# Optimization experiments

Measured on AMD Instinct MI355X. Metric: run time of the kernel, lower is better.

The kernel has to match this reference:

```python
import jax, jax.numpy as jnp
import numpy as np

B, S, C, T = 256, 128, 64, 60
ENC, COL, RNN, ATT, ACT, TYP = 512, 512, 512, 512, 128, 64
NPROD, NTYPE = 97, 32
LS, PTEMP, CTEMP = 0.2, 1.0, 1.0
NEG = -1e9


def setup_inputs() -> dict:
    key = jax.random.key(0)
    ks = jax.random.split(key, 24)
    enc = jax.random.normal(ks[0], (B, S, ENC), jnp.float32)
    col_enc = jax.random.normal(ks[1], (B, C, COL), jnp.float32)
    enc_lens = jax.random.randint(ks[2], (B,), 1, S + 1)
    col_lens = jax.random.randint(ks[3], (B,), 1, C + 1)
    action_kind = jax.random.randint(ks[4], (B, T), 0, 3)  # 0=ApplyRule,1=Reduce,2=SelectColumn
    tgt_lens = jax.random.randint(ks[5], (B,), 1, T + 1)
    prod_ids = jax.random.randint(ks[6], (B, T), 0, NPROD)
    col_ids = jax.random.randint(ks[7], (B, T), 0, C) % col_lens[:, None]
    parent_prod = jax.random.randint(ks[8], (B, T), 0, NPROD)
    parent_type = jax.random.randint(ks[9], (B, T), 0, NTYPE)
    parent_time = jax.random.randint(ks[10], (B, T), 0, T) % jnp.maximum(jnp.arange(T), 1)[None, :]
    g = lambda k, shp: jax.random.normal(k, shp, jnp.float32) * 0.02
    IN = ACT + ATT + ACT + TYP + RNN  # a_tm1 | att_tm1 | parent_prod | parent_type | parent_h
    return dict(
        enc=enc, col_enc=col_enc, enc_lens=enc_lens, col_lens=col_lens,
        action_kind=action_kind, tgt_lens=tgt_lens, prod_ids=prod_ids,
        col_ids=col_ids, parent_prod=parent_prod, parent_type=parent_type,
        parent_time=parent_time,
        prod_embed=g(ks[11], (NPROD + 1, ACT)),
        type_embed=g(ks[12], (NTYPE, TYP)),
        b_lin=jnp.zeros((NPROD + 1,), jnp.float32),
        W_ih=g(ks[13], (IN, 4 * RNN)), W_hh=g(ks[14], (RNN, 4 * RNN)),
        b_lstm=jnp.zeros((4 * RNN,), jnp.float32),
        W_att_q=g(ks[15], (RNN, ENC)),
        W_att_vec=g(ks[16], (ENC + RNN, ATT)),
        W_r1=g(ks[17], (ATT, 4 * ATT)), b_r1=jnp.zeros((4 * ATT,), jnp.float32),
        W_r2=g(ks[18], (4 * ATT, ACT)), b_r2=jnp.zeros((ACT,), jnp.float32),
        W_col_in=g(ks[19], (COL, ACT)),
        W_ptr=g(ks[20], (ATT, COL)),
        w_mem=g(ks[21], (ATT, 1)),
    )


def reference(enc, col_enc, enc_lens, col_lens, action_kind, tgt_lens, prod_ids,
              col_ids, parent_prod, parent_type, parent_time,
              prod_embed, type_embed, b_lin, W_ih, W_hh, b_lstm,
              W_att_q, W_att_vec, W_r1, b_r1, W_r2, b_r2,
              W_col_in, W_ptr, w_mem):
    enc_mask = jnp.arange(S)[None, :] < enc_lens[:, None]   # [B,S]
    col_valid = jnp.arange(C)[None, :] < col_lens[:, None]  # [B,C]
    col_in_embed = jnp.einsum('bcd,da->bca', col_enc, W_col_in)  # column_rnn_input, [B,C,ACT]

    # previous-step actions (a_{t-1}); dummy zeros at t=0 (x is zeroed there anyway)
    shift = lambda a: jnp.concatenate([jnp.zeros_like(a[:, :1]), a[:, :-1]], axis=1)
    kind_p, pid_p, cid_p = shift(action_kind), shift(prod_ids), shift(col_ids)

    def scan_step(carry, xs):
        h, c, att, hist, appear, acc = carry
        t, kp, pp, cp, kind, pid, cid, fprod, ftype, ptime = xs
        # --- prep step input ---
        prev_valid = (t - 1) < tgt_lens
        e_rule = prod_embed[jnp.where(kp == 1, NPROD, pp)]                      # [B,ACT]
        e_col = jnp.take_along_axis(col_in_embed, cp[:, None, None], axis=1)[:, 0]
        a_embed = jnp.where((kp == 2)[:, None], e_col, e_rule)
        a_embed = jnp.where(prev_valid[:, None], a_embed, 0.0)
        parent_h = hist[ptime, jnp.arange(B)]                                   # [B,RNN]
        x = jnp.concatenate([a_embed, att, prod_embed[fprod], type_embed[ftype], parent_h], axis=-1)
        x = jnp.where(t == 0, 0.0, x)
        # --- LSTMCell (torch gate order i,f,g,o) ---
        gates = x @ W_ih + h @ W_hh + b_lstm
        i, f, g_, o = jnp.split(gates, 4, axis=-1)
        c_new = jax.nn.sigmoid(f) * c + jax.nn.sigmoid(i) * jnp.tanh(g_)
        h_new = jax.nn.sigmoid(o) * jnp.tanh(c_new)
        # --- attention over encoder ---
        scores = jnp.einsum('bd,bsd->bs', h_new @ W_att_q, enc)
        scores = jnp.where(enc_mask, scores, NEG)
        ctx = jnp.einsum('bs,bsd->bd', jax.nn.softmax(scores, axis=-1), enc)
        att_new = jnp.tanh(jnp.concatenate([ctx, h_new], axis=-1) @ W_att_vec)
        # --- production readout (tied output embedding) ---
        emb_q = jnp.tanh(att_new @ W_r1 + b_r1) @ W_r2 + b_r2
        rule_lp = jax.nn.log_softmax((emb_q @ prod_embed.T + b_lin) / PTEMP, axis=-1)
        # --- pointer net over columns with memory gate ---
        gate = jax.nn.sigmoid(att_new @ w_mem)                                  # [B,1]
        w_c = jnp.einsum('bd,bcd->bc', att_new @ W_ptr, col_enc)
        weights = w_c * appear * gate + w_c * (1.0 - appear) * (1.0 - gate)
        weights = jnp.where(col_valid, weights, NEG) / CTEMP
        col_lp = jax.nn.log_softmax(weights, axis=-1)
        # --- per-example log prob of gold action ---
        valid = t < tgt_lens
        lp_rule = jnp.take_along_axis(rule_lp, jnp.where(kind == 1, NPROD, pid)[:, None], axis=1)[:, 0]
        lp_col_raw = jnp.take_along_axis(col_lp, cid[:, None], axis=1)[:, 0]
        col_sum = jnp.sum(jnp.where(col_valid, col_lp, 0.0), axis=-1)
        lp_col = (1.0 - LS) * lp_col_raw + LS * col_sum / col_lens
        lp = jnp.where(kind == 2, lp_col, lp_rule)
        acc = acc + jnp.where(valid, lp, 0.0)
        # --- state updates (appear mask updated after use, matching torch) ---
        appear = jnp.maximum(appear, ((kind == 2) & valid)[:, None] * jax.nn.one_hot(cid, C, dtype=appear.dtype))
        hist = hist.at[t].set(h_new)
        return (h_new, c_new, att_new, hist, appear, acc), None

    carry0 = (
        jnp.zeros((B, RNN), jnp.float32), jnp.zeros((B, RNN), jnp.float32),
        jnp.zeros((B, ATT), jnp.float32), jnp.zeros((T, B, RNN), jnp.float32),
        jnp.zeros((B, C), jnp.float32), jnp.zeros((B,), jnp.float32),
    )
    xs = (jnp.arange(T), kind_p.T, pid_p.T, cid_p.T, action_kind.T, prod_ids.T,
          col_ids.T, parent_prod.T, parent_type.T, parent_time.T)
    (_, _, _, _, _, acc), _ = jax.lax.scan(scan_step, carry0, xs)
    return -jnp.mean(acc)
```

## Files before the change

### kernel.cpp

```cpp
#include <hip/hip_runtime.h>
#include <math.h>

#define NB 256
#define NS 128
#define NCOL 64
#define NT 60
#define DENC 512
#define DRNN 512
#define DATT 512
#define DACT 128
#define DTYP 64
#define DG 2048
#define NEGV (-1e9f)
#define NBH 131072
#define NROW 15360
#define RPW 576
#define NRP 2624

typedef unsigned short ushort_t;
typedef __attribute__((ext_vector_type(8))) short short8;
typedef __attribute__((ext_vector_type(4))) float f32x4;

__device__ __forceinline__ float sigf(float x) { return 1.0f / (1.0f + __expf(-x)); }
__device__ __forceinline__ float tanhfast(float x) {
  x = fminf(fmaxf(x, -15.0f), 15.0f);
  float e = __expf(-2.0f * x);
  return (1.0f - e) / (1.0f + e);
}
__device__ __forceinline__ ushort_t f2bf(float f) {
  union { float f; unsigned u; } v; v.f = f;
  unsigned r = v.u + 0x7fffu + ((v.u >> 16) & 1u);
  return (ushort_t)(r >> 16);
}
__device__ __forceinline__ float bf2f(ushort_t b) {
  union { unsigned u; float f; } v; v.u = ((unsigned)b) << 16; return v.f;
}
__device__ __forceinline__ void ld8(const float* p, float* d) {
  f32x4 x = *(const f32x4*)p, y = *(const f32x4*)(p + 4);
  d[0]=x[0]; d[1]=x[1]; d[2]=x[2]; d[3]=x[3];
  d[4]=y[0]; d[5]=y[1]; d[6]=y[2]; d[7]=y[3];
}
__device__ __forceinline__ short8 cvt8(const float* p) {
  f32x4 x = *(const f32x4*)p, y = *(const f32x4*)(p + 4);
  short8 r;
  r[0]=(short)f2bf(x[0]); r[1]=(short)f2bf(x[1]); r[2]=(short)f2bf(x[2]); r[3]=(short)f2bf(x[3]);
  r[4]=(short)f2bf(y[0]); r[5]=(short)f2bf(y[1]); r[6]=(short)f2bf(y[2]); r[7]=(short)f2bf(y[3]);
  return r;
}

__global__ __launch_bounds__(256) void zero_kernel(float* __restrict__ p, int n) {
  int i = blockIdx.x * 256 + threadIdx.x;
  if (i < n) p[i] = 0.0f;
}

__global__ __launch_bounds__(256) void cvt_bf16_kernel(const float* __restrict__ src,
    ushort_t* __restrict__ dst, int n8)
{
  int i = blockIdx.x * 256 + threadIdx.x;
  if (i < n8) *(short8*)&dst[(size_t)i * 8] = cvt8(src + (size_t)i * 8);
}

__global__ __launch_bounds__(256) void pack_w(const float* __restrict__ src,
    ushort_t* __restrict__ dst, int Ksub, int Nsub, int Ntot, int K0, int N0, int ldsrc)
{
  int idx = blockIdx.x * 256 + threadIdx.x;
  if (idx >= Ksub * Nsub) return;
  int k = idx / Nsub, n = idx - k * Nsub;
  int gk = K0 + k;
  dst[((size_t)(gk >> 3) * Ntot + (N0 + n)) * 8 + (gk & 7)] =
      f2bf(src[(size_t)k * ldsrc + n]);
}

__global__ __launch_bounds__(256) void pack_wT(const float* __restrict__ W,
    ushort_t* __restrict__ dst)
{
  int idx = blockIdx.x * 256 + threadIdx.x;
  if (idx >= 512 * 512) return;
  int r = idx >> 9, d = idx & 511;
  dst[((size_t)(d >> 3) * 512 + r) * 8 + (d & 7)] = f2bf(W[(size_t)r * 512 + d]);
}

__global__ __launch_bounds__(256) void r2p_kernel(const float* __restrict__ W_r2,
    const float* __restrict__ prod_embed, const float* __restrict__ b_r2,
    const float* __restrict__ b_lin, ushort_t* __restrict__ Wr2p,
    float* __restrict__ bias2)
{
  int idx = blockIdx.x * 256 + threadIdx.x;
  if (idx >= 2049 * 98) return;
  int k = idx / 98, j = idx - k * 98;
  const float* pe = prod_embed + (size_t)j * DACT;
  if (k < 2048) {
    const float* wr = W_r2 + (size_t)k * DACT;
    float a = 0.f;
    #pragma unroll 8
    for (int d = 0; d < DACT; ++d) a = fmaf(wr[d], pe[d], a);
    Wr2p[((size_t)(k >> 3) * 128 + j) * 8 + (k & 7)] = f2bf(a);
  } else {
    float a = b_lin[j];
    #pragma unroll 8
    for (int d = 0; d < DACT; ++d) a = fmaf(b_r2[d], pe[d], a);
    bias2[j] = a;
  }
}

__global__ __launch_bounds__(64) void appear_kernel(const int* __restrict__ action_kind,
    const int* __restrict__ tgt_lens, const int* __restrict__ col_ids,
    float* __restrict__ appear_all)
{
  int b = blockIdx.x, c = threadIdx.x;
  float ap = 0.f;
  int tl = tgt_lens[b];
  for (int t = 0; t < NT; ++t) {
    appear_all[((size_t)t * NB + b) * 64 + c] = ap;
    if (t < tl && action_kind[b * NT + t] == 2 && col_ids[b * NT + t] == c) ap = 1.f;
  }
}

__global__ __launch_bounds__(256) void gemm_bf16(
    const float* __restrict__ A1, int lda1,
    const ushort_t* __restrict__ Bp, ushort_t* __restrict__ Cb, int ldc,
    int N, int K)
{
  __shared__ short As[2][4096];
  __shared__ short Bs[2][4096];
  const int tid = threadIdx.x;
  const int lane = tid & 63, w = tid >> 6;
  const int wr = w >> 1, wc = w & 1;
  const int mBase = blockIdx.y * 64, nBase = blockIdx.x * 64;
  const int nt = K >> 6;
  f32x4 ra0[2], ra1[2];
  short8 rb[2];
  auto issue = [&](int kt) {
    #pragma unroll
    for (int s = 0; s < 2; ++s) {
      int slot = tid + s * 256;
      int kc = slot >> 6, m = slot & 63;
      int k0 = (kt << 6) + kc * 8;
      const float* p = A1 + (size_t)(mBase + m) * lda1 + k0;
      ra0[s] = *(const f32x4*)p;
      ra1[s] = *(const f32x4*)(p + 4);
      rb[s] = *(const short8*)(Bp + ((size_t)(k0 >> 3) * N + nBase + m) * 8);
    }
  };
  auto store = [&](int buf) {
    #pragma unroll
    for (int s = 0; s < 2; ++s) {
      int slot = tid + s * 256;
      short8 av;
      av[0]=(short)f2bf(ra0[s][0]); av[1]=(short)f2bf(ra0[s][1]);
      av[2]=(short)f2bf(ra0[s][2]); av[3]=(short)f2bf(ra0[s][3]);
      av[4]=(short)f2bf(ra1[s][0]); av[5]=(short)f2bf(ra1[s][1]);
      av[6]=(short)f2bf(ra1[s][2]); av[7]=(short)f2bf(ra1[s][3]);
      *(short8*)&As[buf][slot * 8] = av;
      *(short8*)&Bs[buf][slot * 8] = rb[s];
    }
  };
  f32x4 z4 = {0.f,0.f,0.f,0.f};
  f32x4 acc[2][2] = {{z4,z4},{z4,z4}};
  issue(0); store(0);
  __syncthreads();
  int cur = 0;
  for (int kt = 0; kt < nt; ++kt) {
    bool more = (kt + 1 < nt);
    if (more) issue(kt + 1);
    #pragma unroll
    for (int kk = 0; kk < 2; ++kk) {
      int ko = kk * 4 + (lane >> 4);
      short8 af[2], bfr[2];
      #pragma unroll
      for (int f = 0; f < 2; ++f) {
        int row = wr * 32 + f * 16 + (lane & 15);
        af[f] = *(const short8*)&As[cur][(ko * 64 + row) * 8];
        int col = wc * 32 + f * 16 + (lane & 15);
        bfr[f] = *(const short8*)&Bs[cur][(ko * 64 + col) * 8];
      }
      #pragma unroll
      for (int i = 0; i < 2; ++i)
        #pragma unroll
        for (int j = 0; j < 2; ++j)
          acc[i][j] = __builtin_amdgcn_mfma_f32_16x16x32_bf16(af[i], bfr[j], acc[i][j], 0, 0, 0);
    }
    if (more) store(cur ^ 1);
    __syncthreads();
    cur ^= 1;
  }
  #pragma unroll
  for (int i = 0; i < 2; ++i)
    #pragma unroll
    for (int j = 0; j < 2; ++j)
      #pragma unroll
      for (int r = 0; r < 4; ++r) {
        int row = mBase + wr * 32 + i * 16 + (lane >> 4) * 4 + r;
        int col = nBase + wc * 32 + j * 16 + (lane & 15);
        Cb[(size_t)row * ldc + col] = f2bf(acc[i][j][r]);
      }
}

template <class FA, class FB, class FE>
__device__ __forceinline__ void gemm_core(char* smem, FA loadA, FB loadB,
    int ktBeg, int ktEnd, FE epi)
{
  short* As = (short*)smem;
  short* Bs = (short*)smem + 8192;
  const int tid = threadIdx.x;
  const int lane = tid & 63, w = tid >> 6;
  const int wr = w >> 1, wc = w & 1;
  f32x4 z4 = {0.f,0.f,0.f,0.f};
  f32x4 acc[2][2] = {{z4,z4},{z4,z4}};
  short8 pa[2], pb[2];
  auto issue = [&](int kt) {
    #pragma unroll
    for (int s = 0; s < 2; ++s) {
      int slot = tid + s * 256;
      int kc = slot >> 6;
      int k = (kt << 6) + (kc << 3);
      pa[s] = loadA(k);
      pb[s] = loadB(slot & 63, k);
    }
  };
  auto store = [&](int buf) {
    #pragma unroll
    for (int s = 0; s < 2; ++s) {
      int slot = tid + s * 256;
      *(short8*)&As[buf * 4096 + slot * 8] = pa[s];
      *(short8*)&Bs[buf * 4096 + slot * 8] = pb[s];
    }
  };
  issue(ktBeg); store(0);
  __syncthreads();
  int cur = 0;
  for (int kt = ktBeg; kt < ktEnd; ++kt) {
    bool more = (kt + 1 < ktEnd);
    if (more) issue(kt + 1);
    #pragma unroll
    for (int kk = 0; kk < 2; ++kk) {
      int ko = kk * 4 + (lane >> 4);
      short8 af[2], bfr[2];
      #pragma unroll
      for (int f = 0; f < 2; ++f) {
        int row = wr * 32 + f * 16 + (lane & 15);
        af[f] = *(const short8*)&As[cur * 4096 + (ko * 64 + row) * 8];
        int col = wc * 32 + f * 16 + (lane & 15);
        bfr[f] = *(const short8*)&Bs[cur * 4096 + (ko * 64 + col) * 8];
      }
      #pragma unroll
      for (int i = 0; i < 2; ++i)
        #pragma unroll
        for (int j = 0; j < 2; ++j)
          acc[i][j] = __builtin_amdgcn_mfma_f32_16x16x32_bf16(af[i], bfr[j], acc[i][j], 0, 0, 0);
    }
    if (more) store(cur ^ 1);
    __syncthreads();
    cur ^= 1;
  }
  #pragma unroll
  for (int i = 0; i < 2; ++i)
    #pragma unroll
    for (int j = 0; j < 2; ++j)
      #pragma unroll
      for (int r = 0; r < 4; ++r) {
        int rl = wr * 32 + i * 16 + (lane >> 4) * 4 + r;
        int cl = wc * 32 + j * 16 + (lane & 15);
        epi(rl, cl, acc[i][j][r]);
      }
}

__global__ __launch_bounds__(256) void k1_gates(
    const int* __restrict__ action_kind, const int* __restrict__ tgt_lens,
    const int* __restrict__ prod_ids, const int* __restrict__ col_ids,
    const int* __restrict__ parent_prod, const int* __restrict__ parent_type,
    const int* __restrict__ parent_time,
    const float* __restrict__ prod_embed, const float* __restrict__ type_embed,
    const ushort_t* __restrict__ WpG, const ushort_t* __restrict__ colin_b,
    const ushort_t* __restrict__ att_all, const ushort_t* __restrict__ hist_u,
    float* __restrict__ gates0, float* __restrict__ gates1, int t)
{
  __shared__ __align__(16) char smem[32768];
  const int tid = threadIdx.x;
  const int nb = blockIdx.x, mb = blockIdx.y, ks = blockIdx.z;
  const int mBase = mb * 64, nBase = nb * 64;
  const int b = mBase + (tid & 63);
  int kp = action_kind[b * NT + t - 1];
  int pp = prod_ids[b * NT + t - 1];
  int cp = col_ids[b * NT + t - 1];
  bool pv = (t - 1) < tgt_lens[b];
  int fp = parent_prod[b * NT + t];
  int ft = parent_type[b * NT + t];
  int ptm = parent_time[b * NT + t];
  const ushort_t* hist_prev = hist_u + (size_t)(t - 1) * NBH;
  const ushort_t* att_prev = att_all + (size_t)(t - 1) * NB * DATT;
  auto loadA = [&](int k) -> short8 {
    short8 z = {0,0,0,0,0,0,0,0};
    if (k < 128) {
      if (!pv) return z;
      if (kp == 2) return *(const short8*)(colin_b + ((size_t)(b * NCOL + cp) * DACT + k));
      int row = (kp == 1) ? 97 : pp;
      return cvt8(prod_embed + (size_t)row * DACT + k);
    } else if (k < 640) {
      return *(const short8*)(att_prev + (size_t)b * DATT + (k - 128));
    } else if (k < 768) {
      return cvt8(prod_embed + (size_t)fp * DACT + (k - 640));
    } else if (k < 832) {
      return cvt8(type_embed + (size_t)ft * DTYP + (k - 768));
    } else if (k < 1344) {
      return *(const short8*)(hist_u + (size_t)ptm * NBH + (size_t)b * DRNN + (k - 832));
    } else {
      return *(const short8*)(hist_prev + (size_t)b * DRNN + (k - 1344));
    }
  };
  auto loadB = [&](int n, int k) -> short8 {
    return *(const short8*)(WpG + ((size_t)(k >> 3) * DG + nBase + n) * 8);
  };
  float* gp = ks ? gates1 : gates0;
  auto epi = [&](int rl, int cl, float v) {
    gp[(size_t)(mBase + rl) * DG + nBase + cl] = v;
  };
  gemm_core(smem, loadA, loadB, ks ? 15 : 0, ks ? 29 : 15, epi);
}

struct SmemK23 { float hq[DRNN]; float ml[4][2]; float cs[4][DENC]; };
__global__ __launch_bounds__(256) void k23_lstm_attn(
    const float* __restrict__ g0, const float* __restrict__ g1,
    const float* __restrict__ b_lstm, float* __restrict__ cst,
    ushort_t* __restrict__ hist_t,
    const ushort_t* __restrict__ encWq, const float* __restrict__ enc,
    const int* __restrict__ enc_lens, ushort_t* __restrict__ ctxb)
{
  __shared__ __align__(16) SmemK23 s;
  int b = blockIdx.x, tid = threadIdx.x;
  #pragma unroll
  for (int r = 0; r < 2; ++r) {
    int j = tid + r * 256;
    const float* p0 = g0 + (size_t)b * DG;
    const float* p1 = g1 + (size_t)b * DG;
    float gi = p0[j]        + p1[j]        + b_lstm[j];
    float gf = p0[512 + j]  + p1[512 + j]  + b_lstm[512 + j];
    float gg = p0[1024 + j] + p1[1024 + j] + b_lstm[1024 + j];
    float go = p0[1536 + j] + p1[1536 + j] + b_lstm[1536 + j];
    size_t ix = (size_t)b * DRNN + j;
    float cn = sigf(gf) * cst[ix] + sigf(gi) * tanhfast(gg);
    float hn = sigf(go) * tanhfast(cn);
    cst[ix] = cn;
    hist_t[ix] = f2bf(hn);
    s.hq[j] = hn;
  }
  __syncthreads();
  int w = tid >> 6, lane = tid & 63;
  int el = enc_lens[b];
  float q[8];
  #pragma unroll
  for (int j = 0; j < 8; ++j) q[j] = s.hq[lane * 8 + j];
  float m = -1e30f, lr = 0.f;
  float cacc[8];
  #pragma unroll
  for (int j = 0; j < 8; ++j) cacc[j] = 0.f;
  const ushort_t* eWb = encWq + (size_t)b * NS * DENC + lane * 8;
  const float* eb = enc + (size_t)b * NS * DENC + lane * 8;
  for (int sI = w; sI < el; sI += 4) {
    short8 xr = *(const short8*)(eWb + (size_t)sI * DENC);
    float ev[8];
    ld8(eb + (size_t)sI * DENC, ev);
    float d = 0.f;
    #pragma unroll
    for (int j = 0; j < 8; ++j) d = fmaf(bf2f((ushort_t)xr[j]), q[j], d);
    #pragma unroll
    for (int off = 32; off > 0; off >>= 1) d += __shfl_xor(d, off);
    float mn = fmaxf(m, d);
    float rr = __expf(m - mn), p = __expf(d - mn);
    lr = lr * rr + p;
    #pragma unroll
    for (int j = 0; j < 8; ++j) cacc[j] = cacc[j] * rr + p * ev[j];
    m = mn;
  }
  if (lane == 0) { s.ml[w][0] = m; s.ml[w][1] = lr; }
  #pragma unroll
  for (int j = 0; j < 8; ++j) s.cs[w][lane * 8 + j] = cacc[j];
  __syncthreads();
  float M = fmaxf(fmaxf(s.ml[0][0], s.ml[1][0]), fmaxf(s.ml[2][0], s.ml[3][0]));
  float f0 = __expf(s.ml[0][0] - M), f1 = __expf(s.ml[1][0] - M);
  float f2 = __expf(s.ml[2][0] - M), f3 = __expf(s.ml[3][0] - M);
  float invL = 1.f / (f0 * s.ml[0][1] + f1 * s.ml[1][1] + f2 * s.ml[2][1] + f3 * s.ml[3][1]);
  #pragma unroll
  for (int rep = 0; rep < 2; ++rep) {
    int d = tid + rep * 256;
    ctxb[(size_t)b * DENC + d] =
        f2bf((f0 * s.cs[0][d] + f1 * s.cs[1][d] + f2 * s.cs[2][d] + f3 * s.cs[3][d]) * invL);
  }
}

__global__ __launch_bounds__(256) void k4_attvec(const ushort_t* __restrict__ ctxb,
    const ushort_t* __restrict__ hist_t, const ushort_t* __restrict__ WpV,
    ushort_t* __restrict__ att_all, int t)
{
  __shared__ __align__(16) char smem[32768];
  const int tid = threadIdx.x;
  const int mBase = blockIdx.y * 64, nBase = blockIdx.x * 64;
  const int b = mBase + (tid & 63);
  auto loadA = [&](int k) -> short8 {
    if (k < 512) return *(const short8*)(ctxb + (size_t)b * DENC + k);
    return *(const short8*)(hist_t + (size_t)b * DRNN + (k - 512));
  };
  auto loadB = [&](int n, int k) -> short8 {
    return *(const short8*)(WpV + ((size_t)(k >> 3) * 512 + nBase + n) * 8);
  };
  auto epi = [&](int rl, int cl, float v) {
    att_all[((size_t)t * NB + mBase + rl) * DATT + nBase + cl] = f2bf(tanhfast(v));
  };
  gemm_core(smem, loadA, loadB, 0, 16, epi);
}

__global__ __launch_bounds__(256) void kbig_r1ptr(const ushort_t* __restrict__ att_all,
    const ushort_t* __restrict__ WpRP, const float* __restrict__ b_r1,
    ushort_t* __restrict__ r1c, ushort_t* __restrict__ ptrq_all,
    float* __restrict__ gate_all, int rowBase)
{
  __shared__ __align__(16) char smem[32768];
  const int tid = threadIdx.x;
  const int mBase = blockIdx.y * 64, nBase = blockIdx.x * 64;
  const size_t grow = (size_t)rowBase + mBase + (tid & 63);
  auto loadA = [&](int k) -> short8 {
    return *(const short8*)(att_all + grow * DATT + k);
  };
  auto loadB = [&](int n, int k) -> short8 {
    return *(const short8*)(WpRP + ((size_t)(k >> 3) * NRP + nBase + n) * 8);
  };
  auto epi = [&](int rl, int cl, float v) {
    int col = nBase + cl;
    size_t gr = (size_t)rowBase + mBase + rl;
    if (col < 2048)      r1c[(size_t)(mBase + rl) * DG + col] = f2bf(tanhfast(v + b_r1[col]));
    else if (col < 2560) ptrq_all[gr * RPW + (col - 2048)] = f2bf(v);
    else if (col == 2560) gate_all[gr] = v;
  };
  gemm_core(smem, loadA, loadB, 0, 8, epi);
}

__global__ __launch_bounds__(256) void klogits(const ushort_t* __restrict__ r1c,
    const ushort_t* __restrict__ Wr2p, float* __restrict__ logits_all, int rowBase)
{
  __shared__ __align__(16) char smem[32768];
  const int tid = threadIdx.x;
  const int mBase = blockIdx.y * 64, nBase = blockIdx.x * 64;
  auto loadA = [&](int k) -> short8 {
    return *(const short8*)(r1c + (size_t)(mBase + (tid & 63)) * DG + k);
  };
  auto loadB = [&](int n, int k) -> short8 {
    return *(const short8*)(Wr2p + ((size_t)(k >> 3) * 128 + nBase + n) * 8);
  };
  auto epi = [&](int rl, int cl, float v) {
    logits_all[((size_t)rowBase + mBase + rl) * 128 + nBase + cl] = v;
  };
  gemm_core(smem, loadA, loadB, 0, 32, epi);
}

__global__ __launch_bounds__(256) void kwc(const ushort_t* __restrict__ ptrq_all,
    const ushort_t* __restrict__ colenc_b, float* __restrict__ w_c_all)
{
  __shared__ __align__(16) char smem[32768];
  const int tid = threadIdx.x;
  const int b = blockIdx.x;
  const int tt = tid & 63;
  auto loadA = [&](int k) -> short8 {
    short8 z = {0,0,0,0,0,0,0,0};
    if (tt >= NT) return z;
    return *(const short8*)(ptrq_all + ((size_t)tt * NB + b) * RPW + k);
  };
  auto loadB = [&](int n, int k) -> short8 {
    return *(const short8*)(colenc_b + ((size_t)b * NCOL + n) * 512 + k);
  };
  auto epi = [&](int rl, int cl, float v) {
    if (rl < NT) w_c_all[((size_t)rl * NB + b) * 64 + cl] = v;
  };
  gemm_core(smem, loadA, loadB, 0, 8, epi);
}

__global__ __launch_bounds__(64) void kfinal(
    const float* __restrict__ logits_all, const float* __restrict__ bias2,
    const float* __restrict__ w_c_all, const float* __restrict__ gate_all,
    const float* __restrict__ appear_all, const int* __restrict__ col_lens,
    const int* __restrict__ tgt_lens, const int* __restrict__ action_kind,
    const int* __restrict__ prod_ids, const int* __restrict__ col_ids,
    float* __restrict__ loss_tb)
{
  int row = blockIdx.x;
  int t = row >> 8, b = row & 255;
  int c = threadIdx.x;
  float l0 = logits_all[(size_t)row * 128 + c] + bias2[c];
  float l1 = (c + 64 < 98) ? logits_all[(size_t)row * 128 + 64 + c] + bias2[64 + c] : -1e30f;
  float m = fmaxf(l0, l1);
  #pragma unroll
  for (int off = 32; off > 0; off >>= 1) m = fmaxf(m, __shfl_down(m, off));
  m = __shfl(m, 0);
  float sv = __expf(l0 - m) + ((c + 64 < 98) ? __expf(l1 - m) : 0.f);
  #pragma unroll
  for (int off = 32; off > 0; off >>= 1) sv += __shfl_down(sv, off);
  sv = __shfl(sv, 0);
  float lseR = m + __logf(sv);
  int clen = col_lens[b];
  float gate = sigf(gate_all[row]);
  float ap = appear_all[(size_t)row * 64 + c];
  float wc = w_c_all[(size_t)row * 64 + c];
  float wv = wc * (ap * gate + (1.f - ap) * (1.f - gate));
  wv = (c < clen) ? wv : NEGV;
  float m2 = wv;
  #pragma unroll
  for (int off = 32; off > 0; off >>= 1) m2 = fmaxf(m2, __shfl_down(m2, off));
  m2 = __shfl(m2, 0);
  float s2 = __expf(wv - m2);
  #pragma unroll
  for (int off = 32; off > 0; off >>= 1) s2 += __shfl_down(s2, off);
  s2 = __shfl(s2, 0);
  float lse2 = m2 + __logf(s2);
  float csum = (c < clen) ? (wv - lse2) : 0.f;
  #pragma unroll
  for (int off = 32; off > 0; off >>= 1) csum += __shfl_down(csum, off);
  int kind = action_kind[b * NT + t];
  int cid = col_ids[b * NT + t];
  float wcid = __shfl(wv, cid);
  if (c == 0) {
    int pid = prod_ids[b * NT + t];
    bool valid = t < tgt_lens[b];
    int gj = (kind == 1) ? 97 : pid;
    float lgj = logits_all[(size_t)row * 128 + gj] + bias2[gj];
    float lp_rule = lgj - lseR;
    float lp_col = 0.8f * (wcid - lse2) + 0.2f * csum / (float)clen;
    float lp = (kind == 2) ? lp_col : lp_rule;
    loss_tb[row] = valid ? lp : 0.f;
  }
}

__global__ __launch_bounds__(256) void loss_reduce(const float* __restrict__ loss_tb,
                                                   float* __restrict__ out) {
  int tid = threadIdx.x;
  float v = 0.f;
  for (int k = 0; k < NT; ++k) v += loss_tb[(size_t)k * NB + tid];
  #pragma unroll
  for (int off = 32; off > 0; off >>= 1) v += __shfl_down(v, off);
  __shared__ float part[4];
  if ((tid & 63) == 0) part[tid >> 6] = v;
  __syncthreads();
  if (tid == 0) out[0] = -(part[0] + part[1] + part[2] + part[3]) * (1.0f / NB);
}

extern "C" void kernel_launch(void* const* d_in, const int* in_sizes, int n_in,
                              void* d_out, int out_size, void* d_ws, size_t ws_size,
                              hipStream_t stream) {
  const float* enc         = (const float*)d_in[0];
  const float* col_enc     = (const float*)d_in[1];
  const int*   enc_lens    = (const int*)d_in[2];
  const int*   col_lens    = (const int*)d_in[3];
  const int*   action_kind = (const int*)d_in[4];
  const int*   tgt_lens    = (const int*)d_in[5];
  const int*   prod_ids    = (const int*)d_in[6];
  const int*   col_ids     = (const int*)d_in[7];
  const int*   parent_prod = (const int*)d_in[8];
  const int*   parent_type = (const int*)d_in[9];
  const int*   parent_time = (const int*)d_in[10];
  const float* prod_embed  = (const float*)d_in[11];
  const float* type_embed  = (const float*)d_in[12];
  const float* b_lin       = (const float*)d_in[13];
  const float* W_ih        = (const float*)d_in[14];
  const float* W_hh        = (const float*)d_in[15];
  const float* b_lstm      = (const float*)d_in[16];
  const float* W_att_q     = (const float*)d_in[17];
  const float* W_att_vec   = (const float*)d_in[18];
  const float* W_r1        = (const float*)d_in[19];
  const float* b_r1        = (const float*)d_in[20];
  const float* W_r2        = (const float*)d_in[21];
  const float* b_r2        = (const float*)d_in[22];
  const float* W_col_in    = (const float*)d_in[23];
  const float* W_ptr       = (const float*)d_in[24];
  const float* w_mem       = (const float*)d_in[25];

  float* base = (float*)d_ws;
  size_t o = 0;
  float* cst    = base + o; o += 131072;
  float* gates0 = base + o; o += 524288;
  float* gates1 = base + o; o += 524288;
  int zeroN = (int)o;
  ushort_t* hist_u = (ushort_t*)(base + o); o += 3932160;
  float* logits_all = (float*)hist_u;
  ushort_t* colin_b = (ushort_t*)(base + o); o += 1048576;
  ushort_t* ctxb    = (ushort_t*)(base + o); o += 65536;
  float* encWq_f    = base + o; o += 8388608;
  ushort_t* encWq   = (ushort_t*)encWq_f;
  ushort_t* colenc_b = (ushort_t*)encWq_f;
  ushort_t* r1c      = (ushort_t*)(encWq_f + 4194304);
  ushort_t* att_all  = (ushort_t*)(base + o); o += 3932160;
  ushort_t* ptrq_all = (ushort_t*)(base + o); o += 4423680;
  float* gate_all    = base + o; o += 15360;
  float* w_c_all     = base + o; o += 983040;
  float* appear_all  = base + o; o += 983040;
  float* loss_tb     = base + o; o += 15360;
  ushort_t* WpG   = (ushort_t*)(base + o); o += 1900544;
  ushort_t* WqTp  = (ushort_t*)(base + o); o += 131072;
  ushort_t* WpV   = (ushort_t*)(base + o); o += 262144;
  ushort_t* WpRP  = (ushort_t*)(base + o); o += 671744;
  ushort_t* WpCI  = (ushort_t*)(base + o); o += 32768;
  ushort_t* Wr2p  = (ushort_t*)(base + o); o += 131072;
  float* bias2    = base + o; o += 128;
  (void)ws_size; (void)in_sizes; (void)n_in; (void)out_size;

  zero_kernel<<<(zeroN + 255) / 256, 256, 0, stream>>>(base, zeroN);
  zero_kernel<<<(671744 + 255) / 256, 256, 0, stream>>>((float*)WpRP, 671744);
  zero_kernel<<<(131072 + 255) / 256, 256, 0, stream>>>((float*)Wr2p, 131072);

  pack_w<<<(1344 * 2048 + 255) / 256, 256, 0, stream>>>(W_ih, WpG, 1344, 2048, 2048, 0, 0, 2048);
  pack_w<<<(512 * 2048 + 255) / 256, 256, 0, stream>>>(W_hh, WpG, 512, 2048, 2048, 1344, 0, 2048);
  pack_wT<<<(512 * 512 + 255) / 256, 256, 0, stream>>>(W_att_q, WqTp);
  pack_w<<<(1024 * 512 + 255) / 256, 256, 0, stream>>>(W_att_vec, WpV, 1024, 512, 512, 0, 0, 512);
  pack_w<<<(512 * 2048 + 255) / 256, 256, 0, stream>>>(W_r1, WpRP, 512, 2048, NRP, 0, 0, 2048);
  pack_w<<<(512 * 512 + 255) / 256, 256, 0, stream>>>(W_ptr, WpRP, 512, 512, NRP, 0, 2048, 512);
  pack_w<<<(512 + 255) / 256, 256, 0, stream>>>(w_mem, WpRP, 512, 1, NRP, 0, 2560, 1);
  pack_w<<<(512 * 128 + 255) / 256, 256, 0, stream>>>(W_col_in, WpCI, 512, 128, 128, 0, 0, 128);
  r2p_kernel<<<(2049 * 98 + 255) / 256, 256, 0, stream>>>(W_r2, prod_embed, b_r2, b_lin, Wr2p, bias2);
  appear_kernel<<<NB, 64, 0, stream>>>(action_kind, tgt_lens, col_ids, appear_all);

  gemm_bf16<<<dim3(2, 256), 256, 0, stream>>>(col_enc, 512, WpCI, colin_b, 128, 128, 512);
  gemm_bf16<<<dim3(8, 512), 256, 0, stream>>>(enc, 512, WqTp, encWq, 512, 512, 512);

  for (int t = 0; t < NT; ++t) {
    ushort_t* hist_t = hist_u + (size_t)t * NBH;
    if (t > 0)
      k1_gates<<<dim3(32, 4, 2), 256, 0, stream>>>(
          action_kind, tgt_lens, prod_ids, col_ids, parent_prod, parent_type,
          parent_time, prod_embed, type_embed, WpG, colin_b, att_all, hist_u,
          gates0, gates1, t);
    k23_lstm_attn<<<NB, 256, 0, stream>>>(gates0, gates1, b_lstm, cst, hist_t,
                                          encWq, enc, enc_lens, ctxb);
    k4_attvec<<<dim3(8, 4), 256, 0, stream>>>(ctxb, hist_t, WpV, att_all, t);
  }

  cvt_bf16_kernel<<<(1048576 + 255) / 256, 256, 0, stream>>>(col_enc, colenc_b, 1048576);
  for (int ch = 0; ch < 4; ++ch) {
    int rowBase = ch * 3840;
    kbig_r1ptr<<<dim3(41, 60), 256, 0, stream>>>(att_all, WpRP, b_r1, r1c,
                                                 ptrq_all, gate_all, rowBase);
    klogits<<<dim3(2, 60), 256, 0, stream>>>(r1c, Wr2p, logits_all, rowBase);
  }
  kwc<<<NB, 256, 0, stream>>>(ptrq_all, colenc_b, w_c_all);
  kfinal<<<NROW, 64, 0, stream>>>(logits_all, bias2, w_c_all, gate_all,
      appear_all, col_lens, tgt_lens, action_kind, prod_ids, col_ids, loss_tb);
  loss_reduce<<<1, 256, 0, stream>>>(loss_tb, (float*)d_out);
}
```

Baseline: 3.496 ms.

## Fuse attention-vector projection into LSTM/attention kernel and split gate GEMM four ways

```diff
diff --git a/kernel.cpp b/kernel.cpp
--- a/kernel.cpp
+++ b/kernel.cpp
@@ -80,6 +80,15 @@
   dst[((size_t)(d >> 3) * 512 + r) * 8 + (d & 7)] = f2bf(W[(size_t)r * 512 + d]);
 }
 
+__global__ __launch_bounds__(256) void pack_wvT(const float* __restrict__ W,
+    ushort_t* __restrict__ dst)
+{
+  int idx = blockIdx.x * 256 + threadIdx.x;
+  if (idx >= 1024 * 512) return;
+  int k = idx >> 9, j = idx & 511;
+  dst[(size_t)j * 1024 + k] = f2bf(W[(size_t)k * 512 + j]);
+}
+
 __global__ __launch_bounds__(256) void r2p_kernel(const float* __restrict__ W_r2,
     const float* __restrict__ prod_embed, const float* __restrict__ b_r2,
     const float* __restrict__ b_lin, ushort_t* __restrict__ Wr2p,
@@ -196,6 +205,59 @@
       }
 }
 
+__global__ __launch_bounds__(256) void gemm_encwq(
+    const float* __restrict__ enc, const ushort_t* __restrict__ WqTp,
+    ushort_t* __restrict__ encWq)
+{
+  __shared__ short Asm[32768];
+  const int tid = threadIdx.x;
+  const int lane = tid & 63, w = tid >> 6;
+  const int wr = w >> 1, wc = w & 1;
+  const int mBase = blockIdx.x * 64;
+  #pragma unroll
+  for (int it = 0; it < 16; ++it) {
+    int o = tid + it * 256;
+    int row = o >> 6, c = o & 63;
+    short8 v = cvt8(enc + (size_t)(mBase + row) * 512 + c * 8);
+    *(short8*)&Asm[row * 512 + ((c ^ (row & 7)) * 8)] = v;
+  }
+  __syncthreads();
+  for (int nt = 0; nt < 8; ++nt) {
+    f32x4 z4 = {0.f,0.f,0.f,0.f};
+    f32x4 acc[2][2] = {{z4,z4},{z4,z4}};
+    #pragma unroll 2
+    for (int kt = 0; kt < 8; ++kt) {
+      #pragma unroll
+      for (int kk = 0; kk < 2; ++kk) {
+        int ko = kt * 8 + kk * 4 + (lane >> 4);
+        short8 af[2], bfr[2];
+        #pragma unroll
+        for (int f = 0; f < 2; ++f) {
+          int row = wr * 32 + f * 16 + (lane & 15);
+          af[f] = *(const short8*)&Asm[row * 512 + ((ko ^ (row & 7)) * 8)];
+          int col = nt * 64 + wc * 32 + f * 16 + (lane & 15);
+          bfr[f] = *(const short8*)(WqTp + ((size_t)ko * 512 + col) * 8);
+        }
+        #pragma unroll
+        for (int i = 0; i < 2; ++i)
+          #pragma unroll
+          for (int j = 0; j < 2; ++j)
+            acc[i][j] = __builtin_amdgcn_mfma_f32_16x16x32_bf16(af[i], bfr[j], acc[i][j], 0, 0, 0);
+      }
+    }
+    #pragma unroll
+    for (int i = 0; i < 2; ++i)
+      #pragma unroll
+      for (int j = 0; j < 2; ++j)
+        #pragma unroll
+        for (int r = 0; r < 4; ++r) {
+          int row = mBase + wr * 32 + i * 16 + (lane >> 4) * 4 + r;
+          int col = nt * 64 + wc * 32 + j * 16 + (lane & 15);
+          encWq[(size_t)row * 512 + col] = f2bf(acc[i][j][r]);
+        }
+  }
+}
+
 template <class FA, class FB, class FE>
 __device__ __forceinline__ void gemm_core(char* smem, FA loadA, FB loadB,
     int ktBeg, int ktEnd, FE epi)
@@ -273,7 +335,8 @@
     const float* __restrict__ prod_embed, const float* __restrict__ type_embed,
     const ushort_t* __restrict__ WpG, const ushort_t* __restrict__ colin_b,
     const ushort_t* __restrict__ att_all, const ushort_t* __restrict__ hist_u,
-    float* __restrict__ gates0, float* __restrict__ gates1, int t)
+    float* __restrict__ gates0, float* __restrict__ gates1,
+    float* __restrict__ gates2, float* __restrict__ gates3, int t)
 {
   __shared__ __align__(16) char smem[32768];
   const int tid = threadIdx.x;
@@ -311,45 +374,51 @@
   auto loadB = [&](int n, int k) -> short8 {
     return *(const short8*)(WpG + ((size_t)(k >> 3) * DG + nBase + n) * 8);
   };
-  float* gp = ks ? gates1 : gates0;
+  float* gp = (ks == 0) ? gates0 : (ks == 1) ? gates1 : (ks == 2) ? gates2 : gates3;
   auto epi = [&](int rl, int cl, float v) {
     gp[(size_t)(mBase + rl) * DG + nBase + cl] = v;
   };
-  gemm_core(smem, loadA, loadB, ks ? 15 : 0, ks ? 29 : 15, epi);
-}
-
-struct SmemK23 { float hq[DRNN]; float ml[4][2]; float cs[4][DENC]; };
-__global__ __launch_bounds__(256) void k23_lstm_attn(
+  const int kb0 = (ks == 0) ? 0 : (ks == 1) ? 8 : (ks == 2) ? 15 : 22;
+  const int kb1 = (ks == 0) ? 8 : (ks == 1) ? 15 : (ks == 2) ? 22 : 29;
+  gemm_core(smem, loadA, loadB, kb0, kb1, epi);
+}
+
+struct SmemK23 { float ctxh[1024]; float ml[4][2]; float cs[4][DENC]; };
+__global__ __launch_bounds__(256) void k23_fused(
     const float* __restrict__ g0, const float* __restrict__ g1,
+    const float* __restrict__ g2, const float* __restrict__ g3,
     const float* __restrict__ b_lstm, float* __restrict__ cst,
     ushort_t* __restrict__ hist_t,
     const ushort_t* __restrict__ encWq, const float* __restrict__ enc,
-    const int* __restrict__ enc_lens, ushort_t* __restrict__ ctxb)
+    const int* __restrict__ enc_lens, const ushort_t* __restrict__ WvT,
+    ushort_t* __restrict__ att_t)
 {
   __shared__ __align__(16) SmemK23 s;
   int b = blockIdx.x, tid = threadIdx.x;
+  const float* p0 = g0 + (size_t)b * DG;
+  const float* p1 = g1 + (size_t)b * DG;
+  const float* p2 = g2 + (size_t)b * DG;
+  const float* p3 = g3 + (size_t)b * DG;
   #pragma unroll
   for (int r = 0; r < 2; ++r) {
     int j = tid + r * 256;
-    const float* p0 = g0 + (size_t)b * DG;
-    const float* p1 = g1 + (size_t)b * DG;
-    float gi = p0[j]        + p1[j]        + b_lstm[j];
-    float gf = p0[512 + j]  + p1[512 + j]  + b_lstm[512 + j];
-    float gg = p0[1024 + j] + p1[1024 + j] + b_lstm[1024 + j];
-    float go = p0[1536 + j] + p1[1536 + j] + b_lstm[1536 + j];
+    float gi = p0[j] + p1[j] + p2[j] + p3[j] + b_lstm[j];
+    float gf = p0[512+j] + p1[512+j] + p2[512+j] + p3[512+j] + b_lstm[512+j];
+    float gg = p0[1024+j] + p1[1024+j] + p2[1024+j] + p3[1024+j] + b_lstm[1024+j];
+    float go = p0[1536+j] + p1[1536+j] + p2[1536+j] + p3[1536+j] + b_lstm[1536+j];
     size_t ix = (size_t)b * DRNN + j;
     float cn = sigf(gf) * cst[ix] + sigf(gi) * tanhfast(gg);
     float hn = sigf(go) * tanhfast(cn);
     cst[ix] = cn;
     hist_t[ix] = f2bf(hn);
-    s.hq[j] = hn;
+    s.ctxh[512 + j] = hn;
   }
   __syncthreads();
   int w = tid >> 6, lane = tid & 63;
   int el = enc_lens[b];
   float q[8];
   #pragma unroll
-  for (int j = 0; j < 8; ++j) q[j] = s.hq[lane * 8 + j];
+  for (int j = 0; j < 8; ++j) q[j] = s.ctxh[512 + lane * 8 + j];
   float m = -1e30f, lr = 0.f;
   float cacc[8];
   #pragma unroll
@@ -383,30 +452,23 @@
   #pragma unroll
   for (int rep = 0; rep < 2; ++rep) {
     int d = tid + rep * 256;
-    ctxb[(size_t)b * DENC + d] =
-        f2bf((f0 * s.cs[0][d] + f1 * s.cs[1][d] + f2 * s.cs[2][d] + f3 * s.cs[3][d]) * invL);
-  }
-}
-
-__global__ __launch_bounds__(256) void k4_attvec(const ushort_t* __restrict__ ctxb,
-    const ushort_t* __restrict__ hist_t, const ushort_t* __restrict__ WpV,
-    ushort_t* __restrict__ att_all, int t)
-{
-  __shared__ __align__(16) char smem[32768];
-  const int tid = threadIdx.x;
-  const int mBase = blockIdx.y * 64, nBase = blockIdx.x * 64;
-  const int b = mBase + (tid & 63);
-  auto loadA = [&](int k) -> short8 {
-    if (k < 512) return *(const short8*)(ctxb + (size_t)b * DENC + k);
-    return *(const short8*)(hist_t + (size_t)b * DRNN + (k - 512));
-  };
-  auto loadB = [&](int n, int k) -> short8 {
-    return *(const short8*)(WpV + ((size_t)(k >> 3) * 512 + nBase + n) * 8);
-  };
-  auto epi = [&](int rl, int cl, float v) {
-    att_all[((size_t)t * NB + mBase + rl) * DATT + nBase + cl] = f2bf(tanhfast(v));
-  };
-  gemm_core(smem, loadA, loadB, 0, 16, epi);
+    s.ctxh[d] = (f0 * s.cs[0][d] + f1 * s.cs[1][d] + f2 * s.cs[2][d] + f3 * s.cs[3][d]) * invL;
+  }
+  __syncthreads();
+  #pragma unroll
+  for (int r = 0; r < 2; ++r) {
+    int j = tid + r * 256;
+    const short8* wp = (const short8*)(WvT + (size_t)j * 1024);
+    float a = 0.f;
+    #pragma unroll 4
+    for (int u = 0; u < 128; ++u) {
+      short8 wv = wp[u];
+      #pragma unroll
+      for (int e = 0; e < 8; ++e)
+        a = fmaf(bf2f((ushort_t)wv[e]), s.ctxh[u * 8 + e], a);
+    }
+    att_t[(size_t)b * DATT + j] = f2bf(tanhfast(a));
+  }
 }
 
 __global__ __launch_bounds__(256) void kbig_r1ptr(const ushort_t* __restrict__ att_all,
@@ -576,11 +638,12 @@
   float* cst    = base + o; o += 131072;
   float* gates0 = base + o; o += 524288;
   float* gates1 = base + o; o += 524288;
+  float* gates2 = base + o; o += 524288;
+  float* gates3 = base + o; o += 524288;
   int zeroN = (int)o;
   ushort_t* hist_u = (ushort_t*)(base + o); o += 3932160;
   float* logits_all = (float*)hist_u;
   ushort_t* colin_b = (ushort_t*)(base + o); o += 1048576;
-  ushort_t* ctxb    = (ushort_t*)(base + o); o += 65536;
   float* encWq_f    = base + o; o += 8388608;
   ushort_t* encWq   = (ushort_t*)encWq_f;
   ushort_t* colenc_b = (ushort_t*)encWq_f;
@@ -593,7 +656,7 @@
   float* loss_tb     = base + o; o += 15360;
   ushort_t* WpG   = (ushort_t*)(base + o); o += 1900544;
   ushort_t* WqTp  = (ushort_t*)(base + o); o += 131072;
-  ushort_t* WpV   = (ushort_t*)(base + o); o += 262144;
+  ushort_t* WvT   = (ushort_t*)(base + o); o += 262144;
   ushort_t* WpRP  = (ushort_t*)(base + o); o += 671744;
   ushort_t* WpCI  = (ushort_t*)(base + o); o += 32768;
   ushort_t* Wr2p  = (ushort_t*)(base + o); o += 131072;
@@ -607,7 +670,7 @@
   pack_w<<<(1344 * 2048 + 255) / 256, 256, 0, stream>>>(W_ih, WpG, 1344, 2048, 2048, 0, 0, 2048);
   pack_w<<<(512 * 2048 + 255) / 256, 256, 0, stream>>>(W_hh, WpG, 512, 2048, 2048, 1344, 0, 2048);
   pack_wT<<<(512 * 512 + 255) / 256, 256, 0, stream>>>(W_att_q, WqTp);
-  pack_w<<<(1024 * 512 + 255) / 256, 256, 0, stream>>>(W_att_vec, WpV, 1024, 512, 512, 0, 0, 512);
+  pack_wvT<<<(1024 * 512 + 255) / 256, 256, 0, stream>>>(W_att_vec, WvT);
   pack_w<<<(512 * 2048 + 255) / 256, 256, 0, stream>>>(W_r1, WpRP, 512, 2048, NRP, 0, 0, 2048);
   pack_w<<<(512 * 512 + 255) / 256, 256, 0, stream>>>(W_ptr, WpRP, 512, 512, NRP, 0, 2048, 512);
   pack_w<<<(512 + 255) / 256, 256, 0, stream>>>(w_mem, WpRP, 512, 1, NRP, 0, 2560, 1);
@@ -616,18 +679,18 @@
   appear_kernel<<<NB, 64, 0, stream>>>(action_kind, tgt_lens, col_ids, appear_all);
 
   gemm_bf16<<<dim3(2, 256), 256, 0, stream>>>(col_enc, 512, WpCI, colin_b, 128, 128, 512);
-  gemm_bf16<<<dim3(8, 512), 256, 0, stream>>>(enc, 512, WqTp, encWq, 512, 512, 512);
+  gemm_encwq<<<512, 256, 0, stream>>>(enc, WqTp, encWq);
 
   for (int t = 0; t < NT; ++t) {
     ushort_t* hist_t = hist_u + (size_t)t * NBH;
     if (t > 0)
-      k1_gates<<<dim3(32, 4, 2), 256, 0, stream>>>(
+      k1_gates<<<dim3(32, 4, 4), 256, 0, stream>>>(
           action_kind, tgt_lens, prod_ids, col_ids, parent_prod, parent_type,
           parent_time, prod_embed, type_embed, WpG, colin_b, att_all, hist_u,
-          gates0, gates1, t);
-    k23_lstm_attn<<<NB, 256, 0, stream>>>(gates0, gates1, b_lstm, cst, hist_t,
-                                          encWq, enc, enc_lens, ctxb);
-    k4_attvec<<<dim3(8, 4), 256, 0, stream>>>(ctxb, hist_t, WpV, att_all, t);
+          gates0, gates1, gates2, gates3, t);
+    k23_fused<<<NB, 256, 0, stream>>>(gates0, gates1, gates2, gates3, b_lstm,
+        cst, hist_t, encWq, enc, enc_lens, WvT,
+        att_all + (size_t)t * NB * DATT);
   }
 
   cvt_bf16_kernel<<<(1048576 + 255) / 256, 256, 0, stream>>>(col_enc, colenc_b, 1048576);
```

Measured after the change: 4.132 ms. 18.2% more time.

## Cache bf16 encoder copy for attention loop and fuse enc projection GEMM

Applied to the files above, without the earlier changes.

```diff
diff --git a/kernel.cpp b/kernel.cpp
--- a/kernel.cpp
+++ b/kernel.cpp
@@ -14,7 +14,7 @@
 #define NEGV (-1e9f)
 #define NBH 131072
 #define NROW 15360
-#define RPW 576
+#define RPW 512
 #define NRP 2624
 
 typedef unsigned short ushort_t;
@@ -34,11 +34,6 @@
 }
 __device__ __forceinline__ float bf2f(ushort_t b) {
   union { unsigned u; float f; } v; v.u = ((unsigned)b) << 16; return v.f;
-}
-__device__ __forceinline__ void ld8(const float* p, float* d) {
-  f32x4 x = *(const f32x4*)p, y = *(const f32x4*)(p + 4);
-  d[0]=x[0]; d[1]=x[1]; d[2]=x[2]; d[3]=x[3];
-  d[4]=y[0]; d[5]=y[1]; d[6]=y[2]; d[7]=y[3];
 }
 __device__ __forceinline__ short8 cvt8(const float* p) {
   f32x4 x = *(const f32x4*)p, y = *(const f32x4*)(p + 4);
@@ -194,6 +189,75 @@
         int col = nBase + wc * 32 + j * 16 + (lane & 15);
         Cb[(size_t)row * ldc + col] = f2bf(acc[i][j][r]);
       }
+}
+
+__global__ __launch_bounds__(256) void gemm_encwq(
+    const float* __restrict__ enc, const ushort_t* __restrict__ WqTp,
+    ushort_t* __restrict__ encWq, ushort_t* __restrict__ enc_b)
+{
+  __shared__ short Asm[32768];
+  const int tid = threadIdx.x;
+  const int lane = tid & 63, w = tid >> 6;
+  const int wr = w >> 1, wc = w & 1;
+  const int mBase = blockIdx.x * 64;
+  #pragma unroll
+  for (int it = 0; it < 16; ++it) {
+    int o = tid + it * 256;
+    int row = o >> 6, c = o & 63;
+    short8 v = cvt8(enc + (size_t)(mBase + row) * 512 + c * 8);
+    *(short8*)&Asm[row * 512 + ((c ^ (row & 7)) * 8)] = v;
+    *(short8*)(enc_b + (size_t)(mBase + row) * 512 + c * 8) = v;
+  }
+  __syncthreads();
+  for (int nt = 0; nt < 8; ++nt) {
+    f32x4 z4 = {0.f,0.f,0.f,0.f};
+    f32x4 acc[2][2] = {{z4,z4},{z4,z4}};
+    short8 bb[2][4];
+    auto loadBf = [&](int kt, short8* dst) {
+      #pragma unroll
+      for (int kk = 0; kk < 2; ++kk)
+        #pragma unroll
+        for (int f = 0; f < 2; ++f) {
+          int ko = kt * 8 + kk * 4 + (lane >> 4);
+          int col = nt * 64 + wc * 32 + f * 16 + (lane & 15);
+          dst[kk * 2 + f] = *(const short8*)(WqTp + ((size_t)ko * 512 + col) * 8);
+        }
+    };
+    loadBf(0, bb[0]);
+    loadBf(1, bb[1]);
+    #pragma unroll
+    for (int kt = 0; kt < 8; ++kt) {
+      short8 cur[4];
+      #pragma unroll
+      for (int i = 0; i < 4; ++i) cur[i] = bb[kt & 1][i];
+      if (kt + 2 < 8) loadBf(kt + 2, bb[kt & 1]);
+      #pragma unroll
+      for (int kk = 0; kk < 2; ++kk) {
+        int ko = kt * 8 + kk * 4 + (lane >> 4);
+        short8 af[2];
+        #pragma unroll
+        for (int f = 0; f < 2; ++f) {
+          int row = wr * 32 + f * 16 + (lane & 15);
+          af[f] = *(const short8*)&Asm[row * 512 + ((ko ^ (row & 7)) * 8)];
+        }
+        #pragma unroll
+        for (int i = 0; i < 2; ++i)
+          #pragma unroll
+          for (int j = 0; j < 2; ++j)
+            acc[i][j] = __builtin_amdgcn_mfma_f32_16x16x32_bf16(af[i], cur[kk * 2 + j], acc[i][j], 0, 0, 0);
+      }
+    }
+    #pragma unroll
+    for (int i = 0; i < 2; ++i)
+      #pragma unroll
+      for (int j = 0; j < 2; ++j)
+        #pragma unroll
+        for (int r = 0; r < 4; ++r) {
+          int row = mBase + wr * 32 + i * 16 + (lane >> 4) * 4 + r;
+          int col = nt * 64 + wc * 32 + j * 16 + (lane & 15);
+          encWq[(size_t)row * 512 + col] = f2bf(acc[i][j][r]);
+        }
+  }
 }
 
 template <class FA, class FB, class FE>
@@ -323,16 +387,16 @@
     const float* __restrict__ g0, const float* __restrict__ g1,
     const float* __restrict__ b_lstm, float* __restrict__ cst,
     ushort_t* __restrict__ hist_t,
-    const ushort_t* __restrict__ encWq, const float* __restrict__ enc,
+    const ushort_t* __restrict__ encWq, const ushort_t* __restrict__ enc_b,
     const int* __restrict__ enc_lens, ushort_t* __restrict__ ctxb)
 {
   __shared__ __align__(16) SmemK23 s;
   int b = blockIdx.x, tid = threadIdx.x;
+  const float* p0 = g0 + (size_t)b * DG;
+  const float* p1 = g1 + (size_t)b * DG;
   #pragma unroll
   for (int r = 0; r < 2; ++r) {
     int j = tid + r * 256;
-    const float* p0 = g0 + (size_t)b * DG;
-    const float* p1 = g1 + (size_t)b * DG;
     float gi = p0[j]        + p1[j]        + b_lstm[j];
     float gf = p0[512 + j]  + p1[512 + j]  + b_lstm[512 + j];
     float gg = p0[1024 + j] + p1[1024 + j] + b_lstm[1024 + j];
@@ -355,11 +419,10 @@
   #pragma unroll
   for (int j = 0; j < 8; ++j) cacc[j] = 0.f;
   const ushort_t* eWb = encWq + (size_t)b * NS * DENC + lane * 8;
-  const float* eb = enc + (size_t)b * NS * DENC + lane * 8;
+  const ushort_t* eb = enc_b + (size_t)b * NS * DENC + lane * 8;
   for (int sI = w; sI < el; sI += 4) {
     short8 xr = *(const short8*)(eWb + (size_t)sI * DENC);
-    float ev[8];
-    ld8(eb + (size_t)sI * DENC, ev);
+    short8 er = *(const short8*)(eb + (size_t)sI * DENC);
     float d = 0.f;
     #pragma unroll
     for (int j = 0; j < 8; ++j) d = fmaf(bf2f((ushort_t)xr[j]), q[j], d);
@@ -369,7 +432,7 @@
     float rr = __expf(m - mn), p = __expf(d - mn);
     lr = lr * rr + p;
     #pragma unroll
-    for (int j = 0; j < 8; ++j) cacc[j] = cacc[j] * rr + p * ev[j];
+    for (int j = 0; j < 8; ++j) cacc[j] = cacc[j] * rr + p * bf2f((ushort_t)er[j]);
     m = mn;
   }
   if (lane == 0) { s.ml[w][0] = m; s.ml[w][1] = lr; }
@@ -580,13 +643,15 @@
   ushort_t* hist_u = (ushort_t*)(base + o); o += 3932160;
   float* logits_all = (float*)hist_u;
   ushort_t* colin_b = (ushort_t*)(base + o); o += 1048576;
-  ushort_t* ctxb    = (ushort_t*)(base + o); o += 65536;
   float* encWq_f    = base + o; o += 8388608;
   ushort_t* encWq   = (ushort_t*)encWq_f;
-  ushort_t* colenc_b = (ushort_t*)encWq_f;
-  ushort_t* r1c      = (ushort_t*)(encWq_f + 4194304);
+  ushort_t* r1c     = (ushort_t*)encWq_f;
+  float* encb_f     = base + o; o += 4194304;
+  ushort_t* enc_b   = (ushort_t*)encb_f;
+  ushort_t* colenc_b = (ushort_t*)encb_f;
   ushort_t* att_all  = (ushort_t*)(base + o); o += 3932160;
-  ushort_t* ptrq_all = (ushort_t*)(base + o); o += 4423680;
+  ushort_t* ptrq_all = (ushort_t*)(base + o); o += 3932160;
+  ushort_t* ctxb     = ptrq_all;
   float* gate_all    = base + o; o += 15360;
   float* w_c_all     = base + o; o += 983040;
   float* appear_all  = base + o; o += 983040;
@@ -616,7 +681,7 @@
   appear_kernel<<<NB, 64, 0, stream>>>(action_kind, tgt_lens, col_ids, appear_all);
 
   gemm_bf16<<<dim3(2, 256), 256, 0, stream>>>(col_enc, 512, WpCI, colin_b, 128, 128, 512);
-  gemm_bf16<<<dim3(8, 512), 256, 0, stream>>>(enc, 512, WqTp, encWq, 512, 512, 512);
+  gemm_encwq<<<512, 256, 0, stream>>>(enc, WqTp, encWq, enc_b);
 
   for (int t = 0; t < NT; ++t) {
     ushort_t* hist_t = hist_u + (size_t)t * NBH;
@@ -626,16 +691,16 @@
           parent_time, prod_embed, type_embed, WpG, colin_b, att_all, hist_u,
           gates0, gates1, t);
     k23_lstm_attn<<<NB, 256, 0, stream>>>(gates0, gates1, b_lstm, cst, hist_t,
-                                          encWq, enc, enc_lens, ctxb);
+                                          encWq, enc_b, enc_lens, ctxb);
     k4_attvec<<<dim3(8, 4), 256, 0, stream>>>(ctxb, hist_t, WpV, att_all, t);
   }
 
   cvt_bf16_kernel<<<(1048576 + 255) / 256, 256, 0, stream>>>(col_enc, colenc_b, 1048576);
-  for (int ch = 0; ch < 4; ++ch) {
-    int rowBase = ch * 3840;
-    kbig_r1ptr<<<dim3(41, 60), 256, 0, stream>>>(att_all, WpRP, b_r1, r1c,
-                                                 ptrq_all, gate_all, rowBase);
-    klogits<<<dim3(2, 60), 256, 0, stream>>>(r1c, Wr2p, logits_all, rowBase);
+  for (int ch = 0; ch < 2; ++ch) {
+    int rowBase = ch * 7680;
+    kbig_r1ptr<<<dim3(41, 120), 256, 0, stream>>>(att_all, WpRP, b_r1, r1c,
+                                                  ptrq_all, gate_all, rowBase);
+    klogits<<<dim3(2, 120), 256, 0, stream>>>(r1c, Wr2p, logits_all, rowBase);
   }
   kwc<<<NB, 256, 0, stream>>>(ptrq_all, colenc_b, w_c_all);
   kfinal<<<NROW, 64, 0, stream>>>(logits_all, bias2, w_c_all, gate_all,
```

New measurement: 3.390 ms. 3.0% less time.
